# Kernel optimization log

Hardware: AMD Instinct MI355X
Metric: run time of the kernel (lower is better)

## Reference

```python
import jax, jax.numpy as jnp
import numpy as np

B, S, I, H = 1024, 1024, 32, 128

def setup_inputs() -> dict:
    key = jax.random.key(0)
    ks = jax.random.split(key, 10)
    def xavier(k, shape):
        fan_in, fan_out = shape
        bound = float(np.sqrt(6.0 / (fan_in + fan_out)))
        return jax.random.uniform(k, shape, jnp.float32, -bound, bound)
    return {
        "x": jax.random.normal(ks[0], (B, S, I), jnp.float32),
        "W_r": xavier(ks[1], (I, H)), "U_r": xavier(ks[2], (H, H)), "b_r": jnp.zeros((H,), jnp.float32),
        "W_z": xavier(ks[3], (I, H)), "U_z": xavier(ks[4], (H, H)), "b_z": jnp.zeros((H,), jnp.float32),
        "W_h": xavier(ks[5], (I, H)), "U_h": xavier(ks[6], (H, H)), "b_h": jnp.zeros((H,), jnp.float32),
    }

def reference(x, W_r, U_r, b_r, W_z, U_z, b_z, W_h, U_h, b_h):
    # x: [B, S, I]. Precompute all input projections in one big GEMM each (math-identical,
    # since x_t @ W is independent across t), then scan the sequential recurrence.
    xz = jnp.einsum('bsi,ih->bsh', x, W_z) + b_z  # [B,S,H]
    xh = jnp.einsum('bsi,ih->bsh', x, W_h) + b_h  # [B,S,H]
    # r_t = sigmoid(x@W_r + h@U_r + b_r) is computed in the original but never used
    # (h_tilde is NOT gated by r), so it has no effect on the output.

    h0 = jnp.zeros((x.shape[0], U_z.shape[0]), x.dtype)  # [B,H]

    def step(h, inp):
        xz_t, xh_t = inp  # each [B,H]
        z = jax.nn.sigmoid(xz_t + h @ U_z)
        hh = jnp.tanh(xh_t + h @ U_h)
        h_new = (1.0 - z) * h + z * hh  # note: swapped vs standard GRU, faithful to source
        return h_new, h_new

    # scan over time: [S,B,H]
    xs = (jnp.swapaxes(xz, 0, 1), jnp.swapaxes(xh, 0, 1))
    h_last, hs = jax.lax.scan(step, h0, xs)
    hidden_seq = jnp.swapaxes(hs, 0, 1)  # [B,S,H]
    return hidden_seq, h_last[None]  # final state keeps leading dim of 1, as in source
```

## Files before the change

### kernel.cpp

```cpp
#include <hip/hip_runtime.h>
#include <hip/hip_bf16.h>

typedef __bf16 bf16x8 __attribute__((ext_vector_type(8)));
typedef float  f32x4  __attribute__((ext_vector_type(4)));
typedef unsigned short u16;
typedef unsigned short u16x4 __attribute__((ext_vector_type(4)));
typedef unsigned long long u64;

#define NB 1024
#define NS 1024
#define NI 32
#define NH 128

__device__ __forceinline__ u64 pack4_bf16(f32x4 v) {
  u16x4 p;
#pragma unroll
  for (int r = 0; r < 4; ++r)
    p[r] = __builtin_bit_cast(u16, (__bf16)v[r]);
  return __builtin_bit_cast(u64, p);
}

__device__ __forceinline__ void lds_barrier() {
  __builtin_amdgcn_sched_barrier(0);
  asm volatile("s_waitcnt lgkmcnt(0)" ::: "memory");
  __builtin_amdgcn_s_barrier();
  asm volatile("" ::: "memory");
  __builtin_amdgcn_sched_barrier(0);
}

__global__ __launch_bounds__(512, 2) void gru_scan(
    const float* __restrict__ x,
    const float* __restrict__ Wz, const float* __restrict__ Uz, const float* __restrict__ bz,
    const float* __restrict__ Wh, const float* __restrict__ Uh, const float* __restrict__ bh,
    float* __restrict__ out)
{
  __shared__ __align__(16) u64    hbuf[2][16][32];
  __shared__ __align__(16) bf16x8 xbuf[2][8][16][4];

  const int tid  = threadIdx.x;
  const int lane = tid & 63;
  const int w    = tid >> 6;
  const int ml   = lane & 15;
  const int g    = lane >> 4;
  const int rb   = blockIdx.x * 16;

  bf16x8 ufrag[2][4];
  bf16x8 wfrag[2];
  f32x4  bias2[2];
  {
    const float* Ug[2] = {Uz, Uh};
    const float* Wg[2] = {Wz, Wh};
    const float* bg[2] = {bz, bh};
    const int n0 = 16 * w + ml;
#pragma unroll
    for (int gate = 0; gate < 2; ++gate) {
#pragma unroll
      for (int kt = 0; kt < 4; ++kt)
#pragma unroll
        for (int j = 0; j < 8; ++j)
          ufrag[gate][kt][j] = (__bf16)Ug[gate][(32 * kt + 8 * g + j) * NH + n0];
#pragma unroll
      for (int j = 0; j < 8; ++j)
        wfrag[gate][j] = (__bf16)Wg[gate][(8 * g + j) * NH + n0];
      const int nb = 16 * w + 4 * g;
#pragma unroll
      for (int r = 0; r < 4; ++r) bias2[gate][r] = bg[gate][nb + r];
    }
  }

  for (int i = tid; i < 16 * 32; i += 512) hbuf[0][i >> 5][i & 31] = 0ULL;

  const int r_st  = tid >> 5;
  const int c8    = tid & 31;
  const int tt_st = c8 >> 2;
  const int un_st = (c8 & 3) ^ (r_st & 3);
  const float* xbase = x + (size_t)(rb + r_st) * (NS * NI) + c8 * 8;

  {
    f32x4 a0 = *(const f32x4*)(xbase);
    f32x4 a1 = *(const f32x4*)(xbase + 4);
    bf16x8 u;
#pragma unroll
    for (int j = 0; j < 4; ++j) { u[j] = (__bf16)a0[j]; u[4 + j] = (__bf16)a1[j]; }
    xbuf[0][tt_st][r_st][un_st] = u;
  }
  __syncthreads();

  const int sw = (ml & 7) << 1;
  int ridx[4];
#pragma unroll
  for (int kt = 0; kt < 4; ++kt) ridx[kt] = (8 * kt + 2 * g) ^ sw;
  const int widx = (4 * w + g) ^ sw;
  const int xidx = g ^ (ml & 3);

  f32x4 hv = {0.f, 0.f, 0.f, 0.f};
  float* optr = out + (size_t)(rb + ml) * NS * NH + 16 * w + 4 * g;

  f32x4 vxa, vxb;
  const float NL2E  = -1.4426950408889634f;
  const float P2L2E =  2.8853900817779268f;
  const f32x4 zero4 = {0.f, 0.f, 0.f, 0.f};

  f32x4 axz, axh;
  {
    bf16x8 xf = xbuf[0][0][ml][xidx];
    axz = __builtin_amdgcn_mfma_f32_16x16x32_bf16(wfrag[0], xf, bias2[0], 0, 0, 0);
    axh = __builtin_amdgcn_mfma_f32_16x16x32_bf16(wfrag[1], xf, bias2[1], 0, 0, 0);
  }

  for (int chunk = 0; chunk < NS / 8; ++chunk) {
    const int  xb   = chunk & 1;
    const bool more = (chunk + 1 < NS / 8);
#pragma unroll
    for (int tt = 0; tt < 8; ++tt) {
      const int t = chunk * 8 + tt;

      if (tt == 0 && more) {
        const float* p = xbase + (size_t)(chunk + 1) * (8 * NI);
        vxa = *(const f32x4*)(p);
        vxb = *(const f32x4*)(p + 4);
      }

      const u64* hrow = &hbuf[t & 1][ml][0];
      bf16x8 hf0 = *(const bf16x8*)(hrow + ridx[0]);
      bf16x8 hf1 = *(const bf16x8*)(hrow + ridx[1]);
      bf16x8 hf2 = *(const bf16x8*)(hrow + ridx[2]);
      bf16x8 hf3 = *(const bf16x8*)(hrow + ridx[3]);

      f32x4 z1 = __builtin_amdgcn_mfma_f32_16x16x32_bf16(ufrag[0][0], hf0, axz,   0, 0, 0);
      f32x4 h1 = __builtin_amdgcn_mfma_f32_16x16x32_bf16(ufrag[1][0], hf0, axh,   0, 0, 0);
      f32x4 z2 = __builtin_amdgcn_mfma_f32_16x16x32_bf16(ufrag[0][2], hf2, zero4, 0, 0, 0);
      f32x4 h2 = __builtin_amdgcn_mfma_f32_16x16x32_bf16(ufrag[1][2], hf2, zero4, 0, 0, 0);
      z1 = __builtin_amdgcn_mfma_f32_16x16x32_bf16(ufrag[0][1], hf1, z1, 0, 0, 0);
      h1 = __builtin_amdgcn_mfma_f32_16x16x32_bf16(ufrag[1][1], hf1, h1, 0, 0, 0);
      z2 = __builtin_amdgcn_mfma_f32_16x16x32_bf16(ufrag[0][3], hf3, z2, 0, 0, 0);
      h2 = __builtin_amdgcn_mfma_f32_16x16x32_bf16(ufrag[1][3], hf3, h2, 0, 0, 0);

      const f32x4 az = z1 + z2;
      const f32x4 ah = h1 + h2;

      f32x4 hn;
#pragma unroll
      for (int r = 0; r < 4; ++r) {
        float ez = __builtin_amdgcn_exp2f(az[r] * NL2E);
        float zz = __builtin_amdgcn_rcpf(1.f + ez);
        float eh = __builtin_amdgcn_exp2f(ah[r] * P2L2E);
        float th = 1.f - 2.f * __builtin_amdgcn_rcpf(1.f + eh);
        hn[r] = __builtin_fmaf(zz, th - hv[r], hv[r]);
      }
      hv = hn;

      hbuf[(t + 1) & 1][ml][widx] = pack4_bf16(hn);

      if (tt == 6 && more) {
        bf16x8 u;
#pragma unroll
        for (int j = 0; j < 4; ++j) { u[j] = (__bf16)vxa[j]; u[4 + j] = (__bf16)vxb[j]; }
        xbuf[xb ^ 1][tt_st][r_st][un_st] = u;
      }

      {
        const int nb_ = (tt == 7) ? (xb ^ 1) : xb;
        const int ntt = (tt + 1) & 7;
        bf16x8 xf = xbuf[nb_][ntt][ml][xidx];
        axz = __builtin_amdgcn_mfma_f32_16x16x32_bf16(wfrag[0], xf, bias2[0], 0, 0, 0);
        axh = __builtin_amdgcn_mfma_f32_16x16x32_bf16(wfrag[1], xf, bias2[1], 0, 0, 0);
      }

      __builtin_nontemporal_store(hn, (f32x4*)optr);
      optr += NH;

      lds_barrier();
    }
  }

  const size_t lbase = (size_t)NB * NS * NH + (size_t)(rb + ml) * NH + 16 * w + 4 * g;
  *(f32x4*)(out + lbase) = hv;
}

extern "C" void kernel_launch(void* const* d_in, const int* in_sizes, int n_in,
                              void* d_out, int out_size, void* d_ws, size_t ws_size,
                              hipStream_t stream) {
  const float* x  = (const float*)d_in[0];
  const float* Wz = (const float*)d_in[4];
  const float* Uz = (const float*)d_in[5];
  const float* bz = (const float*)d_in[6];
  const float* Wh = (const float*)d_in[7];
  const float* Uh = (const float*)d_in[8];
  const float* bh = (const float*)d_in[9];
  float* out = (float*)d_out;

  gru_scan<<<dim3(NB / 16), dim3(512), 0, stream>>>(x, Wz, Uz, bz, Wh, Uh, bh, out);
}
```

Before: 479.1 us.

## Load x directly per lane with register prefetch, drop LDS x staging

Removes the shared-memory x staging buffer. Each lane now loads its own x row slice from global memory two timesteps ahead into registers and converts it to bf16 for the input-projection MFMA. The loop is unrolled by two with ping-pong register sets, and the output store of the previous hidden state is moved ahead of the recurrent MFMAs so it overlaps them. This cuts LDS traffic and the per-chunk staging logic, but adds small per-step global loads that now sit inside the latency-critical loop. Each x element is also loaded redundantly by all 8 waves instead of once per block.

Measured after the change: 581.9 us. +21.4%, slower.

```diff
diff --git a/kernel.cpp b/kernel.cpp
--- a/kernel.cpp
+++ b/kernel.cpp
@@ -15,8 +15,7 @@
 __device__ __forceinline__ u64 pack4_bf16(f32x4 v) {
   u16x4 p;
 #pragma unroll
-  for (int r = 0; r < 4; ++r)
-    p[r] = __builtin_bit_cast(u16, (__bf16)v[r]);
+  for (int r = 0; r < 4; ++r) p[r] = __builtin_bit_cast(u16, (__bf16)v[r]);
   return __builtin_bit_cast(u64, p);
 }
 
@@ -34,8 +33,7 @@
     const float* __restrict__ Wh, const float* __restrict__ Uh, const float* __restrict__ bh,
     float* __restrict__ out)
 {
-  __shared__ __align__(16) u64    hbuf[2][16][32];
-  __shared__ __align__(16) bf16x8 xbuf[2][8][16][4];
+  __shared__ __align__(16) u64 hbuf[2][16][32];
 
   const int tid  = threadIdx.x;
   const int lane = tid & 63;
@@ -70,110 +68,96 @@
 
   for (int i = tid; i < 16 * 32; i += 512) hbuf[0][i >> 5][i & 31] = 0ULL;
 
-  const int r_st  = tid >> 5;
-  const int c8    = tid & 31;
-  const int tt_st = c8 >> 2;
-  const int un_st = (c8 & 3) ^ (r_st & 3);
-  const float* xbase = x + (size_t)(rb + r_st) * (NS * NI) + c8 * 8;
-
-  {
-    f32x4 a0 = *(const f32x4*)(xbase);
-    f32x4 a1 = *(const f32x4*)(xbase + 4);
-    bf16x8 u;
-#pragma unroll
-    for (int j = 0; j < 4; ++j) { u[j] = (__bf16)a0[j]; u[4 + j] = (__bf16)a1[j]; }
-    xbuf[0][tt_st][r_st][un_st] = u;
-  }
-  __syncthreads();
-
   const int sw = (ml & 7) << 1;
   int ridx[4];
 #pragma unroll
   for (int kt = 0; kt < 4; ++kt) ridx[kt] = (8 * kt + 2 * g) ^ sw;
   const int widx = (4 * w + g) ^ sw;
-  const int xidx = g ^ (ml & 3);
+
+  const float NL2E  = -1.4426950408889634f;
+  const float P2L2E =  2.8853900817779268f;
+  const f32x4 zero4 = {0.f, 0.f, 0.f, 0.f};
+
+  const float* xrow = x + (size_t)(rb + ml) * (NS * NI) + 8 * g;
+
+  f32x4 xv0a, xv0b, xv1a, xv1b;
+  f32x4 ax0z, ax0h, ax1z, ax1h;
+
+  {
+    f32x4 t0a = ((const f32x4*)xrow)[0];
+    f32x4 t0b = ((const f32x4*)xrow)[1];
+    xv1a = ((const f32x4*)(xrow + NI))[0];
+    xv1b = ((const f32x4*)(xrow + NI))[1];
+    bf16x8 xf;
+#pragma unroll
+    for (int j = 0; j < 4; ++j) { xf[j] = (__bf16)t0a[j]; xf[4 + j] = (__bf16)t0b[j]; }
+    ax0z = __builtin_amdgcn_mfma_f32_16x16x32_bf16(wfrag[0], xf, bias2[0], 0, 0, 0);
+    ax0h = __builtin_amdgcn_mfma_f32_16x16x32_bf16(wfrag[1], xf, bias2[1], 0, 0, 0);
+  }
 
   f32x4 hv = {0.f, 0.f, 0.f, 0.f};
   float* optr = out + (size_t)(rb + ml) * NS * NH + 16 * w + 4 * g;
 
-  f32x4 vxa, vxb;
-  const float NL2E  = -1.4426950408889634f;
-  const float P2L2E =  2.8853900817779268f;
-  const f32x4 zero4 = {0.f, 0.f, 0.f, 0.f};
+  __syncthreads();
 
-  f32x4 axz, axh;
-  {
-    bf16x8 xf = xbuf[0][0][ml][xidx];
-    axz = __builtin_amdgcn_mfma_f32_16x16x32_bf16(wfrag[0], xf, bias2[0], 0, 0, 0);
-    axh = __builtin_amdgcn_mfma_f32_16x16x32_bf16(wfrag[1], xf, bias2[1], 0, 0, 0);
+#define GRU_STEP(P, T, AXZ_C, AXH_C, AXZ_N, AXH_N, XVA_C, XVB_C, XVA_N, XVB_N, DO_STORE)   \
+  {                                                                                        \
+              \
+    const u64* hrow = &hbuf[P][ml][0];                                                     \
+    bf16x8 hf0 = *(const bf16x8*)(hrow + ridx[0]);                                         \
+    bf16x8 hf1 = *(const bf16x8*)(hrow + ridx[1]);                                         \
+    bf16x8 hf2 = *(const bf16x8*)(hrow + ridx[2]);                                         \
+    bf16x8 hf3 = *(const bf16x8*)(hrow + ridx[3]);                                         \
+                                                 \
+    {                                                                                      \
+      int tf = (T) + 2; if (tf > NS - 1) tf = NS - 1;                                      \
+      const f32x4* xp = (const f32x4*)(xrow + (size_t)tf * NI);                            \
+      XVA_N = xp[0]; XVB_N = xp[1];                                                        \
+    }                                                                                      \
+                       \
+    {                                                                                      \
+      bf16x8 xf;                                                                           \
+      _Pragma("unroll")                                                                    \
+      for (int j = 0; j < 4; ++j) { xf[j] = (__bf16)XVA_C[j]; xf[4+j] = (__bf16)XVB_C[j]; }\
+      AXZ_N = __builtin_amdgcn_mfma_f32_16x16x32_bf16(wfrag[0], xf, bias2[0], 0, 0, 0);    \
+      AXH_N = __builtin_amdgcn_mfma_f32_16x16x32_bf16(wfrag[1], xf, bias2[1], 0, 0, 0);    \
+    }                                                                                      \
+                  \
+    if (DO_STORE) { __builtin_nontemporal_store(hv, (f32x4*)optr); optr += NH; }           \
+                                      \
+    f32x4 z1 = __builtin_amdgcn_mfma_f32_16x16x32_bf16(ufrag[0][0], hf0, AXZ_C, 0, 0, 0);  \
+    f32x4 h1 = __builtin_amdgcn_mfma_f32_16x16x32_bf16(ufrag[1][0], hf0, AXH_C, 0, 0, 0);  \
+    f32x4 z2 = __builtin_amdgcn_mfma_f32_16x16x32_bf16(ufrag[0][2], hf2, zero4, 0, 0, 0);  \
+    f32x4 h2 = __builtin_amdgcn_mfma_f32_16x16x32_bf16(ufrag[1][2], hf2, zero4, 0, 0, 0);  \
+    z1 = __builtin_amdgcn_mfma_f32_16x16x32_bf16(ufrag[0][1], hf1, z1, 0, 0, 0);           \
+    h1 = __builtin_amdgcn_mfma_f32_16x16x32_bf16(ufrag[1][1], hf1, h1, 0, 0, 0);           \
+    z2 = __builtin_amdgcn_mfma_f32_16x16x32_bf16(ufrag[0][3], hf3, z2, 0, 0, 0);           \
+    h2 = __builtin_amdgcn_mfma_f32_16x16x32_bf16(ufrag[1][3], hf3, h2, 0, 0, 0);           \
+    const f32x4 az = z1 + z2;                                                              \
+    const f32x4 ah = h1 + h2;                                                              \
+                                     \
+    f32x4 hn;                                                                              \
+    _Pragma("unroll")                                                                      \
+    for (int r = 0; r < 4; ++r) {                                                          \
+      float ez = __builtin_amdgcn_exp2f(az[r] * NL2E);                                     \
+      float zz = __builtin_amdgcn_rcpf(1.f + ez);                                          \
+      float eh = __builtin_amdgcn_exp2f(ah[r] * P2L2E);                                    \
+      float th = 1.f - 2.f * __builtin_amdgcn_rcpf(1.f + eh);                              \
+      hn[r] = __builtin_fmaf(zz, th - hv[r], hv[r]);                                       \
+    }                                                                                      \
+    hv = hn;                                                                               \
+                                       \
+    hbuf[P ^ 1][ml][widx] = pack4_bf16(hn);                                                \
+    lds_barrier();                                                                         \
   }
 
-  for (int chunk = 0; chunk < NS / 8; ++chunk) {
-    const int  xb   = chunk & 1;
-    const bool more = (chunk + 1 < NS / 8);
-#pragma unroll
-    for (int tt = 0; tt < 8; ++tt) {
-      const int t = chunk * 8 + tt;
-
-      if (tt == 0 && more) {
-        const float* p = xbase + (size_t)(chunk + 1) * (8 * NI);
-        vxa = *(const f32x4*)(p);
-        vxb = *(const f32x4*)(p + 4);
-      }
-
-      const u64* hrow = &hbuf[t & 1][ml][0];
-      bf16x8 hf0 = *(const bf16x8*)(hrow + ridx[0]);
-      bf16x8 hf1 = *(const bf16x8*)(hrow + ridx[1]);
-      bf16x8 hf2 = *(const bf16x8*)(hrow + ridx[2]);
-      bf16x8 hf3 = *(const bf16x8*)(hrow + ridx[3]);
-
-      f32x4 z1 = __builtin_amdgcn_mfma_f32_16x16x32_bf16(ufrag[0][0], hf0, axz,   0, 0, 0);
-      f32x4 h1 = __builtin_amdgcn_mfma_f32_16x16x32_bf16(ufrag[1][0], hf0, axh,   0, 0, 0);
-      f32x4 z2 = __builtin_amdgcn_mfma_f32_16x16x32_bf16(ufrag[0][2], hf2, zero4, 0, 0, 0);
-      f32x4 h2 = __builtin_amdgcn_mfma_f32_16x16x32_bf16(ufrag[1][2], hf2, zero4, 0, 0, 0);
-      z1 = __builtin_amdgcn_mfma_f32_16x16x32_bf16(ufrag[0][1], hf1, z1, 0, 0, 0);
-      h1 = __builtin_amdgcn_mfma_f32_16x16x32_bf16(ufrag[1][1], hf1, h1, 0, 0, 0);
-      z2 = __builtin_amdgcn_mfma_f32_16x16x32_bf16(ufrag[0][3], hf3, z2, 0, 0, 0);
-      h2 = __builtin_amdgcn_mfma_f32_16x16x32_bf16(ufrag[1][3], hf3, h2, 0, 0, 0);
-
-      const f32x4 az = z1 + z2;
-      const f32x4 ah = h1 + h2;
-
-      f32x4 hn;
-#pragma unroll
-      for (int r = 0; r < 4; ++r) {
-        float ez = __builtin_amdgcn_exp2f(az[r] * NL2E);
-        float zz = __builtin_amdgcn_rcpf(1.f + ez);
-        float eh = __builtin_amdgcn_exp2f(ah[r] * P2L2E);
-        float th = 1.f - 2.f * __builtin_amdgcn_rcpf(1.f + eh);
-        hn[r] = __builtin_fmaf(zz, th - hv[r], hv[r]);
-      }
-      hv = hn;
-
-      hbuf[(t + 1) & 1][ml][widx] = pack4_bf16(hn);
-
-      if (tt == 6 && more) {
-        bf16x8 u;
-#pragma unroll
-        for (int j = 0; j < 4; ++j) { u[j] = (__bf16)vxa[j]; u[4 + j] = (__bf16)vxb[j]; }
-        xbuf[xb ^ 1][tt_st][r_st][un_st] = u;
-      }
-
-      {
-        const int nb_ = (tt == 7) ? (xb ^ 1) : xb;
-        const int ntt = (tt + 1) & 7;
-        bf16x8 xf = xbuf[nb_][ntt][ml][xidx];
-        axz = __builtin_amdgcn_mfma_f32_16x16x32_bf16(wfrag[0], xf, bias2[0], 0, 0, 0);
-        axh = __builtin_amdgcn_mfma_f32_16x16x32_bf16(wfrag[1], xf, bias2[1], 0, 0, 0);
-      }
-
-      __builtin_nontemporal_store(hn, (f32x4*)optr);
-      optr += NH;
-
-      lds_barrier();
-    }
+  for (int tp = 0; tp < NS / 2; ++tp) {
+    const int tbase = 2 * tp;
+    GRU_STEP(0, tbase,     ax0z, ax0h, ax1z, ax1h, xv1a, xv1b, xv0a, xv0b, (tp > 0))
+    GRU_STEP(1, tbase + 1, ax1z, ax1h, ax0z, ax0h, xv0a, xv0b, xv1a, xv1b, true)
   }
 
+  __builtin_nontemporal_store(hv, (f32x4*)optr);
   const size_t lbase = (size_t)NB * NS * NH + (size_t)(rb + ml) * NH + 16 * w + 4 * g;
   *(f32x4*)(out + lbase) = hv;
 }
```

## Interleave two independent batch tiles per block to hide recurrence latency

Applied to the files above, without the earlier changes.

Each workgroup now advances two 16-row batch tiles in lockstep, with duplicated LDS buffers for hidden state and inputs, and launches half as many blocks. The goal is to fill the latency of the serial MFMA/transcendental chain per timestep with independent work from the second tile, and to amortize barriers. The cost is fewer active CUs and losing the one-step-ahead prefetch of the input projection, which now sits on each step's critical path.

New measurement: 944.8 us. 1.97x slower.

```diff
diff --git a/kernel.cpp b/kernel.cpp
--- a/kernel.cpp
+++ b/kernel.cpp
@@ -15,8 +15,7 @@
 __device__ __forceinline__ u64 pack4_bf16(f32x4 v) {
   u16x4 p;
 #pragma unroll
-  for (int r = 0; r < 4; ++r)
-    p[r] = __builtin_bit_cast(u16, (__bf16)v[r]);
+  for (int r = 0; r < 4; ++r) p[r] = __builtin_bit_cast(u16, (__bf16)v[r]);
   return __builtin_bit_cast(u64, p);
 }
 
@@ -34,15 +33,15 @@
     const float* __restrict__ Wh, const float* __restrict__ Uh, const float* __restrict__ bh,
     float* __restrict__ out)
 {
-  __shared__ __align__(16) u64    hbuf[2][16][32];
-  __shared__ __align__(16) bf16x8 xbuf[2][8][16][4];
+  __shared__ __align__(16) u64    hbuf[2][2][16][32];
+  __shared__ __align__(16) bf16x8 xbuf[2][2][8][16][4];
 
   const int tid  = threadIdx.x;
   const int lane = tid & 63;
   const int w    = tid >> 6;
   const int ml   = lane & 15;
   const int g    = lane >> 4;
-  const int rb   = blockIdx.x * 16;
+  const int rb   = blockIdx.x * 32;
 
   bf16x8 ufrag[2][4];
   bf16x8 wfrag[2];
@@ -68,21 +67,29 @@
     }
   }
 
-  for (int i = tid; i < 16 * 32; i += 512) hbuf[0][i >> 5][i & 31] = 0ULL;
+  for (int i = tid; i < 2 * 16 * 32; i += 512)
+    hbuf[i >> 9][0][(i >> 5) & 15][i & 31] = 0ULL;
 
   const int r_st  = tid >> 5;
   const int c8    = tid & 31;
   const int tt_st = c8 >> 2;
   const int un_st = (c8 & 3) ^ (r_st & 3);
-  const float* xbase = x + (size_t)(rb + r_st) * (NS * NI) + c8 * 8;
+  const float* xbaseA = x + (size_t)(rb + r_st) * (NS * NI) + c8 * 8;
+  const float* xbaseB = x + (size_t)(rb + 16 + r_st) * (NS * NI) + c8 * 8;
 
   {
-    f32x4 a0 = *(const f32x4*)(xbase);
-    f32x4 a1 = *(const f32x4*)(xbase + 4);
-    bf16x8 u;
-#pragma unroll
-    for (int j = 0; j < 4; ++j) { u[j] = (__bf16)a0[j]; u[4 + j] = (__bf16)a1[j]; }
-    xbuf[0][tt_st][r_st][un_st] = u;
+    f32x4 a0 = *(const f32x4*)(xbaseA);
+    f32x4 a1 = *(const f32x4*)(xbaseA + 4);
+    f32x4 b0 = *(const f32x4*)(xbaseB);
+    f32x4 b1 = *(const f32x4*)(xbaseB + 4);
+    bf16x8 uA, uB;
+#pragma unroll
+    for (int j = 0; j < 4; ++j) {
+      uA[j] = (__bf16)a0[j]; uA[4 + j] = (__bf16)a1[j];
+      uB[j] = (__bf16)b0[j]; uB[4 + j] = (__bf16)b1[j];
+    }
+    xbuf[0][0][tt_st][r_st][un_st] = uA;
+    xbuf[1][0][tt_st][r_st][un_st] = uB;
   }
   __syncthreads();
 
@@ -93,19 +100,85 @@
   const int widx = (4 * w + g) ^ sw;
   const int xidx = g ^ (ml & 3);
 
-  f32x4 hv = {0.f, 0.f, 0.f, 0.f};
-  float* optr = out + (size_t)(rb + ml) * NS * NH + 16 * w + 4 * g;
-
-  f32x4 vxa, vxb;
+  f32x4 hvA = {0.f, 0.f, 0.f, 0.f};
+  f32x4 hvB = {0.f, 0.f, 0.f, 0.f};
+  float* optrA = out + (size_t)(rb + ml) * NS * NH + 16 * w + 4 * g;
+  float* optrB = out + (size_t)(rb + 16 + ml) * NS * NH + 16 * w + 4 * g;
+
+  f32x4 vA0, vA1, vB0, vB1;
   const float NL2E  = -1.4426950408889634f;
   const float P2L2E =  2.8853900817779268f;
   const f32x4 zero4 = {0.f, 0.f, 0.f, 0.f};
 
-  f32x4 axz, axh;
-  {
-    bf16x8 xf = xbuf[0][0][ml][xidx];
-    axz = __builtin_amdgcn_mfma_f32_16x16x32_bf16(wfrag[0], xf, bias2[0], 0, 0, 0);
-    axh = __builtin_amdgcn_mfma_f32_16x16x32_bf16(wfrag[1], xf, bias2[1], 0, 0, 0);
+#define GRU_STEP2(P, XB, TT)                                                               \
+  {                                                                                        \
+    const u64* hrA = &hbuf[0][P][ml][0];                                                   \
+    const u64* hrB = &hbuf[1][P][ml][0];                                                   \
+                           \
+    bf16x8 xfA = xbuf[0][XB][TT][ml][xidx];                                                \
+    bf16x8 xfB = xbuf[1][XB][TT][ml][xidx];                                                \
+    bf16x8 a0 = *(const bf16x8*)(hrA + ridx[0]);                                           \
+    bf16x8 a1 = *(const bf16x8*)(hrA + ridx[1]);                                           \
+    bf16x8 a2 = *(const bf16x8*)(hrA + ridx[2]);                                           \
+    bf16x8 a3 = *(const bf16x8*)(hrA + ridx[3]);                                           \
+    bf16x8 b0 = *(const bf16x8*)(hrB + ridx[0]);                                           \
+    bf16x8 b1 = *(const bf16x8*)(hrB + ridx[1]);                                           \
+    bf16x8 b2 = *(const bf16x8*)(hrB + ridx[2]);                                           \
+    bf16x8 b3 = *(const bf16x8*)(hrB + ridx[3]);                                           \
+                    \
+    f32x4 azA = __builtin_amdgcn_mfma_f32_16x16x32_bf16(wfrag[0], xfA, bias2[0], 0, 0, 0); \
+    f32x4 ahA = __builtin_amdgcn_mfma_f32_16x16x32_bf16(wfrag[1], xfA, bias2[1], 0, 0, 0); \
+    f32x4 azB = __builtin_amdgcn_mfma_f32_16x16x32_bf16(wfrag[0], xfB, bias2[0], 0, 0, 0); \
+    f32x4 ahB = __builtin_amdgcn_mfma_f32_16x16x32_bf16(wfrag[1], xfB, bias2[1], 0, 0, 0); \
+                                           \
+    f32x4 z1A = __builtin_amdgcn_mfma_f32_16x16x32_bf16(ufrag[0][0], a0, azA,   0, 0, 0);  \
+    f32x4 h1A = __builtin_amdgcn_mfma_f32_16x16x32_bf16(ufrag[1][0], a0, ahA,   0, 0, 0);  \
+    f32x4 z2A = __builtin_amdgcn_mfma_f32_16x16x32_bf16(ufrag[0][2], a2, zero4, 0, 0, 0);  \
+    f32x4 h2A = __builtin_amdgcn_mfma_f32_16x16x32_bf16(ufrag[1][2], a2, zero4, 0, 0, 0);  \
+    z1A = __builtin_amdgcn_mfma_f32_16x16x32_bf16(ufrag[0][1], a1, z1A, 0, 0, 0);          \
+    h1A = __builtin_amdgcn_mfma_f32_16x16x32_bf16(ufrag[1][1], a1, h1A, 0, 0, 0);          \
+    z2A = __builtin_amdgcn_mfma_f32_16x16x32_bf16(ufrag[0][3], a3, z2A, 0, 0, 0);          \
+    h2A = __builtin_amdgcn_mfma_f32_16x16x32_bf16(ufrag[1][3], a3, h2A, 0, 0, 0);          \
+                                                                      \
+    f32x4 z1B = __builtin_amdgcn_mfma_f32_16x16x32_bf16(ufrag[0][0], b0, azB,   0, 0, 0);  \
+    f32x4 h1B = __builtin_amdgcn_mfma_f32_16x16x32_bf16(ufrag[1][0], b0, ahB,   0, 0, 0);  \
+    f32x4 z2B = __builtin_amdgcn_mfma_f32_16x16x32_bf16(ufrag[0][2], b2, zero4, 0, 0, 0);  \
+    f32x4 h2B = __builtin_amdgcn_mfma_f32_16x16x32_bf16(ufrag[1][2], b2, zero4, 0, 0, 0);  \
+    z1B = __builtin_amdgcn_mfma_f32_16x16x32_bf16(ufrag[0][1], b1, z1B, 0, 0, 0);          \
+    h1B = __builtin_amdgcn_mfma_f32_16x16x32_bf16(ufrag[1][1], b1, h1B, 0, 0, 0);          \
+    z2B = __builtin_amdgcn_mfma_f32_16x16x32_bf16(ufrag[0][3], b3, z2B, 0, 0, 0);          \
+    h2B = __builtin_amdgcn_mfma_f32_16x16x32_bf16(ufrag[1][3], b3, h2B, 0, 0, 0);          \
+                                        \
+    f32x4 hnA, hnB;                                                                        \
+    {                                                                                      \
+      const f32x4 az = z1A + z2A;                                                          \
+      const f32x4 ah = h1A + h2A;                                                          \
+      _Pragma("unroll")                                                                    \
+      for (int r = 0; r < 4; ++r) {                                                        \
+        float ez = __builtin_amdgcn_exp2f(az[r] * NL2E);                                   \
+        float zz = __builtin_amdgcn_rcpf(1.f + ez);                                        \
+        float eh = __builtin_amdgcn_exp2f(ah[r] * P2L2E);                                  \
+        float th = 1.f - 2.f * __builtin_amdgcn_rcpf(1.f + eh);                            \
+        hnA[r] = __builtin_fmaf(zz, th - hvA[r], hvA[r]);                                  \
+      }                                                                                    \
+    }                                                                                      \
+    hbuf[0][P ^ 1][ml][widx] = pack4_bf16(hnA);                                            \
+    {                                                                                      \
+      const f32x4 az = z1B + z2B;                                                          \
+      const f32x4 ah = h1B + h2B;                                                          \
+      _Pragma("unroll")                                                                    \
+      for (int r = 0; r < 4; ++r) {                                                        \
+        float ez = __builtin_amdgcn_exp2f(az[r] * NL2E);                                   \
+        float zz = __builtin_amdgcn_rcpf(1.f + ez);                                        \
+        float eh = __builtin_amdgcn_exp2f(ah[r] * P2L2E);                                  \
+        float th = 1.f - 2.f * __builtin_amdgcn_rcpf(1.f + eh);                            \
+        hnB[r] = __builtin_fmaf(zz, th - hvB[r], hvB[r]);                                  \
+      }                                                                                    \
+    }                                                                                      \
+    hbuf[1][P ^ 1][ml][widx] = pack4_bf16(hnB);                                            \
+    hvA = hnA; hvB = hnB;                                                                  \
+    __builtin_nontemporal_store(hnA, (f32x4*)optrA); optrA += NH;                          \
+    __builtin_nontemporal_store(hnB, (f32x4*)optrB); optrB += NH;                          \
   }
 
   for (int chunk = 0; chunk < NS / 8; ++chunk) {
@@ -113,69 +186,34 @@
     const bool more = (chunk + 1 < NS / 8);
 #pragma unroll
     for (int tt = 0; tt < 8; ++tt) {
-      const int t = chunk * 8 + tt;
-
       if (tt == 0 && more) {
-        const float* p = xbase + (size_t)(chunk + 1) * (8 * NI);
-        vxa = *(const f32x4*)(p);
-        vxb = *(const f32x4*)(p + 4);
+        const float* pA = xbaseA + (size_t)(chunk + 1) * (8 * NI);
+        const float* pB = xbaseB + (size_t)(chunk + 1) * (8 * NI);
+        vA0 = *(const f32x4*)(pA); vA1 = *(const f32x4*)(pA + 4);
+        vB0 = *(const f32x4*)(pB); vB1 = *(const f32x4*)(pB + 4);
       }
 
-      const u64* hrow = &hbuf[t & 1][ml][0];
-      bf16x8 hf0 = *(const bf16x8*)(hrow + ridx[0]);
-      bf16x8 hf1 = *(const bf16x8*)(hrow + ridx[1]);
-      bf16x8 hf2 = *(const bf16x8*)(hrow + ridx[2]);
-      bf16x8 hf3 = *(const bf16x8*)(hrow + ridx[3]);
-
-      f32x4 z1 = __builtin_amdgcn_mfma_f32_16x16x32_bf16(ufrag[0][0], hf0, axz,   0, 0, 0);
-      f32x4 h1 = __builtin_amdgcn_mfma_f32_16x16x32_bf16(ufrag[1][0], hf0, axh,   0, 0, 0);
-      f32x4 z2 = __builtin_amdgcn_mfma_f32_16x16x32_bf16(ufrag[0][2], hf2, zero4, 0, 0, 0);
-      f32x4 h2 = __builtin_amdgcn_mfma_f32_16x16x32_bf16(ufrag[1][2], hf2, zero4, 0, 0, 0);
-      z1 = __builtin_amdgcn_mfma_f32_16x16x32_bf16(ufrag[0][1], hf1, z1, 0, 0, 0);
-      h1 = __builtin_amdgcn_mfma_f32_16x16x32_bf16(ufrag[1][1], hf1, h1, 0, 0, 0);
-      z2 = __builtin_amdgcn_mfma_f32_16x16x32_bf16(ufrag[0][3], hf3, z2, 0, 0, 0);
-      h2 = __builtin_amdgcn_mfma_f32_16x16x32_bf16(ufrag[1][3], hf3, h2, 0, 0, 0);
-
-      const f32x4 az = z1 + z2;
-      const f32x4 ah = h1 + h2;
-
-      f32x4 hn;
-#pragma unroll
-      for (int r = 0; r < 4; ++r) {
-        float ez = __builtin_amdgcn_exp2f(az[r] * NL2E);
-        float zz = __builtin_amdgcn_rcpf(1.f + ez);
-        float eh = __builtin_amdgcn_exp2f(ah[r] * P2L2E);
-        float th = 1.f - 2.f * __builtin_amdgcn_rcpf(1.f + eh);
-        hn[r] = __builtin_fmaf(zz, th - hv[r], hv[r]);
+      if (tt & 1) { GRU_STEP2(1, xb, tt) } else { GRU_STEP2(0, xb, tt) }
+
+      if (tt == 6 && more) {
+        bf16x8 uA, uB;
+#pragma unroll
+        for (int j = 0; j < 4; ++j) {
+          uA[j] = (__bf16)vA0[j]; uA[4 + j] = (__bf16)vA1[j];
+          uB[j] = (__bf16)vB0[j]; uB[4 + j] = (__bf16)vB1[j];
+        }
+        xbuf[0][xb ^ 1][tt_st][r_st][un_st] = uA;
+        xbuf[1][xb ^ 1][tt_st][r_st][un_st] = uB;
       }
-      hv = hn;
-
-      hbuf[(t + 1) & 1][ml][widx] = pack4_bf16(hn);
-
-      if (tt == 6 && more) {
-        bf16x8 u;
-#pragma unroll
-        for (int j = 0; j < 4; ++j) { u[j] = (__bf16)vxa[j]; u[4 + j] = (__bf16)vxb[j]; }
-        xbuf[xb ^ 1][tt_st][r_st][un_st] = u;
-      }
-
-      {
-        const int nb_ = (tt == 7) ? (xb ^ 1) : xb;
-        const int ntt = (tt + 1) & 7;
-        bf16x8 xf = xbuf[nb_][ntt][ml][xidx];
-        axz = __builtin_amdgcn_mfma_f32_16x16x32_bf16(wfrag[0], xf, bias2[0], 0, 0, 0);
-        axh = __builtin_amdgcn_mfma_f32_16x16x32_bf16(wfrag[1], xf, bias2[1], 0, 0, 0);
-      }
-
-      __builtin_nontemporal_store(hn, (f32x4*)optr);
-      optr += NH;
 
       lds_barrier();
     }
   }
 
-  const size_t lbase = (size_t)NB * NS * NH + (size_t)(rb + ml) * NH + 16 * w + 4 * g;
-  *(f32x4*)(out + lbase) = hv;
+  const size_t lbaseA = (size_t)NB * NS * NH + (size_t)(rb + ml) * NH + 16 * w + 4 * g;
+  const size_t lbaseB = (size_t)NB * NS * NH + (size_t)(rb + 16 + ml) * NH + 16 * w + 4 * g;
+  *(f32x4*)(out + lbaseA) = hvA;
+  *(f32x4*)(out + lbaseB) = hvB;
 }
 
 extern "C" void kernel_launch(void* const* d_in, const int* in_sizes, int n_in,
@@ -190,5 +228,5 @@
   const float* bh = (const float*)d_in[9];
   float* out = (float*)d_out;
 
-  gru_scan<<<dim3(NB / 16), dim3(512), 0, stream>>>(x, Wz, Uz, bz, Wh, Uh, bh, out);
-}
+  gru_scan<<<dim3(NB / 32), dim3(512), 0, stream>>>(x, Wz, Uz, bz, Wh, Uh, bh, out);
+}
```
